# Optimization experiments

Hardware: AMD Instinct MI355X
Metric: run time of the kernel (lower is better)

Reference implementation:

```python
import jax, jax.numpy as jnp
import numpy as np

D_EMBED = 768
N_HEADS = 12
HEAD_DIM = D_EMBED // N_HEADS


def setup_inputs() -> dict:
    key = jax.random.key(0)
    ks = jax.random.split(key, 9)
    B, T, C = 4, 2048, D_EMBED
    s = 1.0 / np.sqrt(C)
    return {
        "x": jax.random.normal(ks[0], (B, T, C), dtype=jnp.float32),
        "Wq": jax.random.normal(ks[1], (C, C), dtype=jnp.float32) * s,
        "bq": jnp.zeros((C,), dtype=jnp.float32),
        "Wk": jax.random.normal(ks[2], (C, C), dtype=jnp.float32) * s,
        "bk": jnp.zeros((C,), dtype=jnp.float32),
        "Wv": jax.random.normal(ks[3], (C, C), dtype=jnp.float32) * s,
        "bv": jnp.zeros((C,), dtype=jnp.float32),
        "Wo": jax.random.normal(ks[4], (C, C), dtype=jnp.float32) * s,
        "bo": jnp.zeros((C,), dtype=jnp.float32),
    }


def reference(x, Wq, bq, Wk, bk, Wv, bv, Wo, bo):
    B, T, C = x.shape
    H, D = N_HEADS, HEAD_DIM
    # projections -> [B, H, T, D]
    q = (x @ Wq + bq).reshape(B, T, H, D).transpose(0, 2, 1, 3)
    k = (x @ Wk + bk).reshape(B, T, H, D).transpose(0, 2, 1, 3)
    v = (x @ Wv + bv).reshape(B, T, H, D).transpose(0, 2, 1, 3)
    # full attention matrix [B, H, T, T] (faithful to manual implementation)
    scores = jnp.einsum('bhqd,bhkd->bhqk', q, k) / jnp.sqrt(jnp.float32(D))
    causal = jnp.tril(jnp.ones((T, T), dtype=bool))
    scores = jnp.where(causal, scores, jnp.float32(-jnp.inf))
    weights = jax.nn.softmax(scores, axis=-1)
    out = jnp.einsum('bhqk,bhkd->bhqd', weights, v)
    out = out.transpose(0, 2, 1, 3).reshape(B, T, C)
    return out @ Wo + bo
```

## Files before the change

kernel.cpp:

```cpp
#include <hip/hip_runtime.h>

#define T_LEN 2048
#define C_DIM 768
#define NH 12
#define HD 64
#define B_SZ 4
#define M_ROWS (B_SZ * T_LEN)
#define WSZ (C_DIM * C_DIM)
#define CH 520

typedef __bf16 bf16x8 __attribute__((ext_vector_type(8)));
typedef float f32x4 __attribute__((ext_vector_type(4)));
typedef float f32x16 __attribute__((ext_vector_type(16)));

__device__ __forceinline__ unsigned short f2bf(float f) {
    union { __bf16 b; unsigned short u; } c;
    c.b = (__bf16)f;
    return c.u;
}

__device__ __forceinline__ float fast_exp2(float x) {
    float r;
    asm("v_exp_f32 %0, %1" : "=v"(r) : "v"(x));
    return r;
}

__device__ __forceinline__ unsigned cvt_pk_bf16(float a, float b) {
    unsigned r;
    asm("v_cvt_pk_bf16_f32 %0, %1, %2" : "=v"(r) : "v"(a), "v"(b));
    return r;
}

__device__ __forceinline__ void perml32_swap(unsigned& a, unsigned& b) {
    asm("v_permlane32_swap_b32 %0, %1" : "+v"(a), "+v"(b));
}

__device__ __forceinline__ void gl2lds16(const void* g, void* l) {
    __builtin_amdgcn_global_load_lds(
        (const __attribute__((address_space(1))) unsigned int*)g,
        (__attribute__((address_space(3))) unsigned int*)l, 16, 0, 0);
}

__global__ __launch_bounds__(256) void conv_x(const float* __restrict__ x,
                                              unsigned short* __restrict__ xb)
{
    const int i = blockIdx.x * 256 + threadIdx.x;
    float4 v = ((const float4*)x)[i];
    ushort4 o;
    o.x = f2bf(v.x); o.y = f2bf(v.y); o.z = f2bf(v.z); o.w = f2bf(v.w);
    ((ushort4*)xb)[i] = o;
}

__global__ __launch_bounds__(256) void conv_wt(
    const float* __restrict__ W0, const float* __restrict__ W1,
    const float* __restrict__ W2, const float* __restrict__ W3,
    unsigned short* __restrict__ WtAll)
{
    __shared__ float tile[32][33];
    const int z = blockIdx.z;
    const float* W = (z == 0) ? W0 : (z == 1) ? W1 : (z == 2) ? W2 : W3;
    unsigned short* out = WtAll + (size_t)z * WSZ;
    const int k0 = blockIdx.x * 32, n0 = blockIdx.y * 32;
    const int r = threadIdx.x >> 3, c4 = (threadIdx.x & 7) * 4;
    float4 v = *(const float4*)&W[(size_t)(k0 + r) * C_DIM + n0 + c4];
    tile[r][c4 + 0] = v.x;
    tile[r][c4 + 1] = v.y;
    tile[r][c4 + 2] = v.z;
    tile[r][c4 + 3] = v.w;
    __syncthreads();
    ushort4 o;
    o.x = f2bf(tile[c4 + 0][r]);
    o.y = f2bf(tile[c4 + 1][r]);
    o.z = f2bf(tile[c4 + 2][r]);
    o.w = f2bf(tile[c4 + 3][r]);
    *(ushort4*)&out[(size_t)(n0 + r) * C_DIM + k0 + c4] = o;
}

template <int BN, int MODE>
__global__ __launch_bounds__(256, 2) void gemm_tile(
    const unsigned short* __restrict__ A, const unsigned short* __restrict__ Wt,
    const float* __restrict__ b0, const float* __restrict__ b1,
    const float* __restrict__ b2,
    unsigned short* __restrict__ qg, unsigned short* __restrict__ kg,
    unsigned short* __restrict__ vtg, float* __restrict__ outF)
{
    constexpr int NFC = BN / 32;
    constexpr int NY = (MODE == 0 ? 2304 : 768) / BN;
    __shared__ __align__(16) unsigned short As[2][128 * 64];
    __shared__ __align__(16) unsigned short Bs[2][BN * 64];

    const int tid = threadIdx.x;
    const int lane = tid & 63, w = tid >> 6;
    const int L15 = lane & 15, quad = lane >> 4;
    const int wm = w >> 1, wn = w & 1;

    const int raw = blockIdx.x;
    const int xcd = raw & 7, i = raw >> 3;
    const int mx = xcd * 8 + i / NY;
    const int ny = i % NY;

    const int lr = lane >> 3;
    const int lg8 = (lane & 7) ^ lr;
    const size_t aBase = (size_t)(mx * 128 + w * 8 + lr) * C_DIM + lg8 * 8;
    const size_t bBase = (size_t)(ny * BN + w * 8 + lr) * C_DIM + lg8 * 8;

    auto stage = [&](int kt, int buf) {
        const size_t ko = (size_t)kt * 64;
#pragma unroll
        for (int c = 0; c < 4; c++)
            gl2lds16(&A[aBase + (size_t)c * 32 * C_DIM + ko],
                     &As[buf][(c * 32 + w * 8) * 64]);
#pragma unroll
        for (int c = 0; c < BN / 32; c++)
            gl2lds16(&Wt[bBase + (size_t)c * 32 * C_DIM + ko],
                     &Bs[buf][(c * 32 + w * 8) * 64]);
    };

    const int sg0 = (quad ^ (L15 & 7)) * 16;
    const int sg1 = ((4 + quad) ^ (L15 & 7)) * 16;
    const int aRowB = (wm * 64 + L15) * 128;
    const int bRowB = (wn * (BN / 2) + L15) * 128;

    f32x4 acc[4][NFC];
#pragma unroll
    for (int fr = 0; fr < 4; fr++)
#pragma unroll
        for (int fc = 0; fc < NFC; fc++) acc[fr][fc] = 0.0f;

    stage(0, 0);
    __syncthreads();

    for (int kt = 0; kt < 12; kt++) {
        const int cur = kt & 1;
        if (kt < 11) stage(kt + 1, cur ^ 1);
        const char* Ac = (const char*)As[cur];
        const char* Bc = (const char*)Bs[cur];
        bf16x8 av[4][2], bv[NFC][2];
#pragma unroll
        for (int fr = 0; fr < 4; fr++)
#pragma unroll
            for (int kh = 0; kh < 2; kh++)
                av[fr][kh] = *(const bf16x8*)(Ac + aRowB + fr * 2048 + (kh ? sg1 : sg0));
#pragma unroll
        for (int fc = 0; fc < NFC; fc++)
#pragma unroll
            for (int kh = 0; kh < 2; kh++)
                bv[fc][kh] = *(const bf16x8*)(Bc + bRowB + fc * 2048 + (kh ? sg1 : sg0));
        __builtin_amdgcn_s_setprio(1);
#pragma unroll
        for (int fr = 0; fr < 4; fr++)
#pragma unroll
            for (int fc = 0; fc < NFC; fc++)
#pragma unroll
                for (int kh = 0; kh < 2; kh++)
                    acc[fr][fc] = __builtin_amdgcn_mfma_f32_16x16x32_bf16(
                        av[fr][kh], bv[fc][kh], acc[fr][fc], 0, 0, 0);
        __builtin_amdgcn_s_setprio(0);
        __syncthreads();
    }

    if (MODE == 0) {
        const int z = (ny * BN) / 768;
        const float* bias = (z == 0) ? b0 : (z == 1) ? b1 : b2;
        const float qs = (z == 0) ? 0.18033688011112042f : 1.0f;
#pragma unroll
        for (int fc = 0; fc < NFC; fc++) {
            const int n = ny * BN + wn * (BN / 2) + fc * 16 + L15;
            const int nl = n - z * 768;
            const int h = nl >> 6, d = nl & 63;
            const float bn = bias[nl];
#pragma unroll
            for (int fr = 0; fr < 4; fr++) {
                const int mB = mx * 128 + wm * 64 + fr * 16 + quad * 4;
                const int b = mB >> 11, tB = mB & (T_LEN - 1);
                if (z < 2) {
                    unsigned short* o = z ? kg : qg;
#pragma unroll
                    for (int r = 0; r < 4; r++)
                        o[(((size_t)(b * NH + h)) * T_LEN + tB + r) * HD + d] =
                            f2bf((acc[fr][fc][r] + bn) * qs);
                } else {
                    ushort4 o4;
                    o4.x = f2bf(acc[fr][fc][0] + bn);
                    o4.y = f2bf(acc[fr][fc][1] + bn);
                    o4.z = f2bf(acc[fr][fc][2] + bn);
                    o4.w = f2bf(acc[fr][fc][3] + bn);
                    *(ushort4*)&vtg[(((size_t)(b * NH + h)) * HD + d) * T_LEN + tB] = o4;
                }
            }
        }
    } else {
#pragma unroll
        for (int fc = 0; fc < NFC; fc++) {
            const int n = ny * BN + wn * (BN / 2) + fc * 16 + L15;
            const float bn = b0[n];
#pragma unroll
            for (int fr = 0; fr < 4; fr++) {
                const int mB = mx * 128 + wm * 64 + fr * 16 + quad * 4;
#pragma unroll
                for (int r = 0; r < 4; r++)
                    outF[(size_t)(mB + r) * C_DIM + n] = acc[fr][fc][r] + bn;
            }
        }
    }
}

__global__ __launch_bounds__(256, 4) void attn_mfma(
    const unsigned short* __restrict__ qg, const unsigned short* __restrict__ kg,
    const unsigned short* __restrict__ vtg, unsigned short* __restrict__ attb)
{
    __shared__ __align__(16) unsigned short Ks[2][8 * CH];
    __shared__ __align__(16) unsigned short Vs[2][8 * CH];
    const int tid = threadIdx.x;
    const int lane = tid & 63, w = tid >> 6;
    const int L15 = lane & 15, L31 = lane & 31;
    const int quad = lane >> 4, r4 = (lane >> 4) & 1, r5 = lane >> 5;

    const int n = blockIdx.x;
    const int bh = n % (B_SZ * NH);
    const int m = n / (B_SZ * NH);
    const int qi = (m & 1) ? (m >> 1) : (15 - (m >> 1));
    const size_t base = (size_t)bh * T_LEN * HD;
    const int q0 = qi * 128;
    const int nk = 2 * qi + 2;
    const int qrow = q0 + w * 32 + L31;

    bf16x8 qf[4];
#pragma unroll
    for (int kc = 0; kc < 4; kc++)
        qf[kc] = *(const bf16x8*)&qg[base + (size_t)qrow * HD + kc * 16 + r5 * 8];

    f32x16 accO[2];
#pragma unroll
    for (int md = 0; md < 2; md++) accO[md] = 0.0f;
    f32x4 lacc = 0.0f;

    auto stage = [&](int kt, int buf) {
        const int ktb = kt * 64;
        gl2lds16(&kg[base + (size_t)(ktb + w * 16 + L15) * HD + quad * 8],
                 &Ks[buf][(2 * w) * CH]);
        gl2lds16(&kg[base + (size_t)(ktb + w * 16 + L15) * HD + 32 + quad * 8],
                 &Ks[buf][(2 * w + 1) * CH]);
        gl2lds16(&vtg[base + (size_t)(w * 16 + L15) * T_LEN + ktb + quad * 8],
                 &Vs[buf][(2 * w) * CH]);
        gl2lds16(&vtg[base + (size_t)(w * 16 + L15) * T_LEN + ktb + 32 + quad * 8],
                 &Vs[buf][(2 * w + 1) * CH]);
    };

    stage(0, 0);
    __syncthreads();

    const int qmaxw = q0 + w * 32 + 31;
    const int qminw = q0 + w * 32;

    for (int kt = 0; kt < nk; kt++) {
        const int cur = kt & 1;
        if (kt + 1 < nk) stage(kt + 1, cur ^ 1);
        const int ktb = kt * 64;
        if (ktb <= qmaxw) {
            f32x16 sa[2];
#pragma unroll
            for (int mi = 0; mi < 2; mi++) {
                sa[mi] = 0.0f;
#pragma unroll
                for (int kc = 0; kc < 4; kc++) {
                    const int ck = mi * 4 + r4 * 2 + (kc >> 1);
                    const int slot = L15 + 16 * ((kc & 1) * 2 + r5);
                    bf16x8 kf = *(const bf16x8*)&Ks[cur][ck * CH + slot * 8];
                    sa[mi] = __builtin_amdgcn_mfma_f32_32x32x16_bf16(
                        kf, qf[kc], sa[mi], 0, 0, 0);
                }
            }
            const bool needmask = (ktb + 63 > qminw);
            bf16x8 pfrag[4];
#pragma unroll
            for (int mi = 0; mi < 2; mi++) {
                float e[16];
#pragma unroll
                for (int g = 0; g < 4; g++) {
#pragma unroll
                    for (int rr = 0; rr < 4; rr++) {
                        float s = sa[mi][g * 4 + rr];
                        if (needmask) {
                            const int key = ktb + mi * 32 + 8 * g + 4 * r5 + rr;
                            s = (key <= qrow) ? s : -1e30f;
                        }
                        e[g * 4 + rr] = fast_exp2(s);
                        lacc[rr] += e[g * 4 + rr];
                    }
                }
#pragma unroll
                for (int h = 0; h < 2; h++) {
                    unsigned a0 = cvt_pk_bf16(e[8 * h + 0], e[8 * h + 1]);
                    unsigned a1 = cvt_pk_bf16(e[8 * h + 2], e[8 * h + 3]);
                    unsigned b0 = cvt_pk_bf16(e[8 * h + 4], e[8 * h + 5]);
                    unsigned b1 = cvt_pk_bf16(e[8 * h + 6], e[8 * h + 7]);
                    perml32_swap(a0, b0);
                    perml32_swap(a1, b1);
                    union { unsigned u[4]; bf16x8 v; } pf;
                    pf.u[0] = a0; pf.u[1] = a1; pf.u[2] = b0; pf.u[3] = b1;
                    pfrag[2 * mi + h] = pf.v;
                }
            }
#pragma unroll
            for (int md = 0; md < 2; md++) {
#pragma unroll
                for (int kc = 0; kc < 4; kc++) {
                    const int cv = md * 4 + r4 * 2 + (kc >> 1);
                    const int slot = L15 + 16 * ((kc & 1) * 2 + r5);
                    bf16x8 vf = *(const bf16x8*)&Vs[cur][cv * CH + slot * 8];
                    accO[md] = __builtin_amdgcn_mfma_f32_32x32x16_bf16(
                        vf, pfrag[kc], accO[md], 0, 0, 0);
                }
            }
        }
        __syncthreads();
    }

    const float l = (lacc[0] + lacc[1]) + (lacc[2] + lacc[3]);
    const float lt = l + __shfl_xor(l, 32, 64);
    const float inv = __builtin_amdgcn_rcpf(lt);
    const int b = bh / NH, h = bh % NH;
    const size_t orow = ((size_t)(b * T_LEN + qrow)) * C_DIM + h * HD;
#pragma unroll
    for (int md = 0; md < 2; md++) {
#pragma unroll
        for (int g = 0; g < 4; g++) {
            uint2 wv;
            wv.x = (unsigned)f2bf(accO[md][g * 4 + 0] * inv) |
                   ((unsigned)f2bf(accO[md][g * 4 + 1] * inv) << 16);
            wv.y = (unsigned)f2bf(accO[md][g * 4 + 2] * inv) |
                   ((unsigned)f2bf(accO[md][g * 4 + 3] * inv) << 16);
            *(uint2*)&attb[orow + md * 32 + 8 * g + 4 * r5] = wv;
        }
    }
}

extern "C" void kernel_launch(void* const* d_in, const int* in_sizes, int n_in,
                              void* d_out, int out_size, void* d_ws, size_t ws_size,
                              hipStream_t stream)
{
    const float* x  = (const float*)d_in[0];
    const float* Wq = (const float*)d_in[1];
    const float* bq = (const float*)d_in[2];
    const float* Wk = (const float*)d_in[3];
    const float* bk = (const float*)d_in[4];
    const float* Wv = (const float*)d_in[5];
    const float* bv = (const float*)d_in[6];
    const float* Wo = (const float*)d_in[7];
    const float* bo = (const float*)d_in[8];
    float* out = (float*)d_out;

    const size_t nMC = (size_t)M_ROWS * C_DIM;
    unsigned short* xb   = (unsigned short*)d_ws;
    unsigned short* Wt   = xb + nMC;
    unsigned short* qg   = Wt + 4 * (size_t)WSZ;
    unsigned short* kg   = qg + nMC;
    unsigned short* vtg  = kg + nMC;
    unsigned short* attb = vtg + nMC;

    conv_x<<<(int)(nMC / 1024), 256, 0, stream>>>(x, xb);
    conv_wt<<<dim3(24, 24, 4), 256, 0, stream>>>(Wq, Wk, Wv, Wo, Wt);
    gemm_tile<192, 0><<<768, 256, 0, stream>>>(xb, Wt, bq, bk, bv,
                                               qg, kg, vtg, nullptr);
    attn_mfma<<<16 * B_SZ * NH, 256, 0, stream>>>(qg, kg, vtg, attb);
    gemm_tile<96, 1><<<512, 256, 0, stream>>>(attb, Wt + 3 * (size_t)WSZ,
                                              bo, bo, bo, nullptr, nullptr,
                                              nullptr, out);
}
```

Before: 213.0 us.

## Split causal attention into balanced key-range chunks with combine pass; use 32x32 MFMA GEMM

Attention work for long query blocks is split across several key-range segments via static tables, so each of the 1920 blocks has similar work. Partial unnormalized outputs and row sums go into scratch that reuses the output buffer and the no-longer-needed bf16 x buffer, and a separate combine kernel sums them and normalizes. The causal diagonal tile now skips the upper-half QK and PV MFMAs. The projection GEMMs switch from 16x16x32 to 32x32x16 MFMA tiles with new LDS indexing. This adds an extra kernel launch plus scratch traffic, and partials are rounded to bf16 before summation.

New measurement: 212.2 us. Within noise of the previous version (-0.4%).

```diff
diff --git a/kernel.cpp b/kernel.cpp
--- a/kernel.cpp
+++ b/kernel.cpp
@@ -39,6 +39,13 @@
     __builtin_amdgcn_global_load_lds(
         (const __attribute__((address_space(1))) unsigned int*)g,
         (__attribute__((address_space(3))) unsigned int*)l, 16, 0, 0);
+}
+
+__device__ __forceinline__ float bf_lo(unsigned u) {
+    union { unsigned u; float f; } c; c.u = u << 16; return c.f;
+}
+__device__ __forceinline__ float bf_hi(unsigned u) {
+    union { unsigned u; float f; } c; c.u = u & 0xFFFF0000u; return c.f;
 }
 
 __global__ __launch_bounds__(256) void conv_x(const float* __restrict__ x,
@@ -84,15 +91,17 @@
     unsigned short* __restrict__ qg, unsigned short* __restrict__ kg,
     unsigned short* __restrict__ vtg, float* __restrict__ outF)
 {
-    constexpr int NFC = BN / 32;
+    constexpr int NT = 3;
+    constexpr int MT = (MODE == 0) ? 2 : 1;
     constexpr int NY = (MODE == 0 ? 2304 : 768) / BN;
     __shared__ __align__(16) unsigned short As[2][128 * 64];
     __shared__ __align__(16) unsigned short Bs[2][BN * 64];
 
     const int tid = threadIdx.x;
     const int lane = tid & 63, w = tid >> 6;
-    const int L15 = lane & 15, quad = lane >> 4;
-    const int wm = w >> 1, wn = w & 1;
+    const int L31 = lane & 31, r5 = lane >> 5;
+    const int wm = (MODE == 0) ? (w >> 1) : w;
+    const int wn = (MODE == 0) ? (w & 1) : 0;
 
     const int raw = blockIdx.x;
     const int xcd = raw & 7, i = raw >> 3;
@@ -116,16 +125,15 @@
                      &Bs[buf][(c * 32 + w * 8) * 64]);
     };
 
-    const int sg0 = (quad ^ (L15 & 7)) * 16;
-    const int sg1 = ((4 + quad) ^ (L15 & 7)) * 16;
-    const int aRowB = (wm * 64 + L15) * 128;
-    const int bRowB = (wn * (BN / 2) + L15) * 128;
-
-    f32x4 acc[4][NFC];
-#pragma unroll
-    for (int fr = 0; fr < 4; fr++)
-#pragma unroll
-        for (int fc = 0; fc < NFC; fc++) acc[fr][fc] = 0.0f;
+    const int ax7 = L31 & 7;
+    const int aRowB = (wm * (MT * 32) + L31) * 128;
+    const int bRowB = (wn * 96 + L31) * 128;
+
+    f32x16 acc[MT][NT];
+#pragma unroll
+    for (int mt = 0; mt < MT; mt++)
+#pragma unroll
+        for (int nt = 0; nt < NT; nt++) acc[mt][nt] = 0.0f;
 
     stage(0, 0);
     __syncthreads();
@@ -135,26 +143,28 @@
         if (kt < 11) stage(kt + 1, cur ^ 1);
         const char* Ac = (const char*)As[cur];
         const char* Bc = (const char*)Bs[cur];
-        bf16x8 av[4][2], bv[NFC][2];
-#pragma unroll
-        for (int fr = 0; fr < 4; fr++)
-#pragma unroll
-            for (int kh = 0; kh < 2; kh++)
-                av[fr][kh] = *(const bf16x8*)(Ac + aRowB + fr * 2048 + (kh ? sg1 : sg0));
-#pragma unroll
-        for (int fc = 0; fc < NFC; fc++)
-#pragma unroll
-            for (int kh = 0; kh < 2; kh++)
-                bv[fc][kh] = *(const bf16x8*)(Bc + bRowB + fc * 2048 + (kh ? sg1 : sg0));
+        bf16x8 av[MT][4], bv[NT][4];
+#pragma unroll
+        for (int mt = 0; mt < MT; mt++)
+#pragma unroll
+            for (int ks = 0; ks < 4; ks++)
+                av[mt][ks] = *(const bf16x8*)(Ac + aRowB + mt * 32 * 128 +
+                                              (((2 * ks + r5) ^ ax7) * 16));
+#pragma unroll
+        for (int nt = 0; nt < NT; nt++)
+#pragma unroll
+            for (int ks = 0; ks < 4; ks++)
+                bv[nt][ks] = *(const bf16x8*)(Bc + bRowB + nt * 32 * 128 +
+                                              (((2 * ks + r5) ^ ax7) * 16));
         __builtin_amdgcn_s_setprio(1);
 #pragma unroll
-        for (int fr = 0; fr < 4; fr++)
-#pragma unroll
-            for (int fc = 0; fc < NFC; fc++)
-#pragma unroll
-                for (int kh = 0; kh < 2; kh++)
-                    acc[fr][fc] = __builtin_amdgcn_mfma_f32_16x16x32_bf16(
-                        av[fr][kh], bv[fc][kh], acc[fr][fc], 0, 0, 0);
+        for (int ks = 0; ks < 4; ks++)
+#pragma unroll
+            for (int mt = 0; mt < MT; mt++)
+#pragma unroll
+                for (int nt = 0; nt < NT; nt++)
+                    acc[mt][nt] = __builtin_amdgcn_mfma_f32_32x32x16_bf16(
+                        av[mt][ks], bv[nt][ks], acc[mt][nt], 0, 0, 0);
         __builtin_amdgcn_s_setprio(0);
         __syncthreads();
     }
@@ -164,51 +174,75 @@
         const float* bias = (z == 0) ? b0 : (z == 1) ? b1 : b2;
         const float qs = (z == 0) ? 0.18033688011112042f : 1.0f;
 #pragma unroll
-        for (int fc = 0; fc < NFC; fc++) {
-            const int n = ny * BN + wn * (BN / 2) + fc * 16 + L15;
+        for (int nt = 0; nt < NT; nt++) {
+            const int n = ny * BN + wn * 96 + nt * 32 + L31;
             const int nl = n - z * 768;
             const int h = nl >> 6, d = nl & 63;
             const float bn = bias[nl];
 #pragma unroll
-            for (int fr = 0; fr < 4; fr++) {
-                const int mB = mx * 128 + wm * 64 + fr * 16 + quad * 4;
-                const int b = mB >> 11, tB = mB & (T_LEN - 1);
+            for (int mt = 0; mt < MT; mt++) {
+                const int mB = mx * 128 + wm * (MT * 32) + mt * 32;
+                const int b = mB >> 11, tBb = mB & (T_LEN - 1);
                 if (z < 2) {
                     unsigned short* o = z ? kg : qg;
 #pragma unroll
-                    for (int r = 0; r < 4; r++)
-                        o[(((size_t)(b * NH + h)) * T_LEN + tB + r) * HD + d] =
-                            f2bf((acc[fr][fc][r] + bn) * qs);
+                    for (int reg = 0; reg < 16; reg++) {
+                        const int t = tBb + (reg & 3) + 8 * (reg >> 2) + 4 * r5;
+                        o[(((size_t)(b * NH + h)) * T_LEN + t) * HD + d] =
+                            f2bf((acc[mt][nt][reg] + bn) * qs);
+                    }
                 } else {
-                    ushort4 o4;
-                    o4.x = f2bf(acc[fr][fc][0] + bn);
-                    o4.y = f2bf(acc[fr][fc][1] + bn);
-                    o4.z = f2bf(acc[fr][fc][2] + bn);
-                    o4.w = f2bf(acc[fr][fc][3] + bn);
-                    *(ushort4*)&vtg[(((size_t)(b * NH + h)) * HD + d) * T_LEN + tB] = o4;
+#pragma unroll
+                    for (int g = 0; g < 4; g++) {
+                        const int t0 = tBb + 8 * g + 4 * r5;
+                        ushort4 o4;
+                        o4.x = f2bf(acc[mt][nt][g * 4 + 0] + bn);
+                        o4.y = f2bf(acc[mt][nt][g * 4 + 1] + bn);
+                        o4.z = f2bf(acc[mt][nt][g * 4 + 2] + bn);
+                        o4.w = f2bf(acc[mt][nt][g * 4 + 3] + bn);
+                        *(ushort4*)&vtg[(((size_t)(b * NH + h)) * HD + d) * T_LEN + t0] = o4;
+                    }
                 }
             }
         }
     } else {
 #pragma unroll
-        for (int fc = 0; fc < NFC; fc++) {
-            const int n = ny * BN + wn * (BN / 2) + fc * 16 + L15;
+        for (int nt = 0; nt < NT; nt++) {
+            const int n = ny * BN + nt * 32 + L31;
             const float bn = b0[n];
 #pragma unroll
-            for (int fr = 0; fr < 4; fr++) {
-                const int mB = mx * 128 + wm * 64 + fr * 16 + quad * 4;
-#pragma unroll
-                for (int r = 0; r < 4; r++)
-                    outF[(size_t)(mB + r) * C_DIM + n] = acc[fr][fc][r] + bn;
+            for (int reg = 0; reg < 16; reg++) {
+                const int m = mx * 128 + w * 32 + (reg & 3) + 8 * (reg >> 2) + 4 * r5;
+                outF[(size_t)m * C_DIM + n] = acc[0][nt][reg] + bn;
             }
         }
     }
 }
 
-__global__ __launch_bounds__(256, 4) void attn_mfma(
+__global__ __launch_bounds__(256, 4) void attn_part(
     const unsigned short* __restrict__ qg, const unsigned short* __restrict__ kg,
-    const unsigned short* __restrict__ vtg, unsigned short* __restrict__ attb)
-{
+    const unsigned short* __restrict__ vtg, unsigned short* __restrict__ attb,
+    float* __restrict__ pOa, unsigned short* __restrict__ pOb,
+    float* __restrict__ pL)
+{
+    static const unsigned char Uqs[40] = {
+        15,15,15,15,14,14,11,11,11,10, 7, 7, 3,
+        14,14,13,13,13,13,12,12,10,10, 9, 9, 6, 6,
+        12,12, 9, 8, 8, 8, 5, 5, 2, 4, 4, 1, 0};
+    static const unsigned char Uk0[40] = {
+         0, 8,16,24, 0, 8, 0, 8,16, 0, 0, 8, 0,
+        16,23, 0, 7,14,21, 0, 7, 8,15, 0, 7, 0, 7,
+        14,20,14, 0, 6,12, 0, 6, 0, 0, 5, 0, 0};
+    static const unsigned char Uk1[40] = {
+         8,16,24,32, 8,16, 8,16,24, 8, 8,16, 8,
+        23,30, 7,14,21,28, 7,14,15,22, 7,14, 7,14,
+        20,26,20, 6,12,18, 6,12, 6, 5,10, 4, 2};
+    static const unsigned char Useg[40] = {
+         0, 1, 2, 3, 0, 1, 0, 1, 2, 0, 0, 1, 0,
+         2, 3, 0, 1, 2, 3, 0, 1, 1, 2, 0, 1, 0, 1,
+         2, 3, 2, 0, 1, 2, 0, 1, 0, 0, 1, 0, 0};
+    static const unsigned char SB[12] = {0,2,4,6,8,11,14,17,20,24,28,32};
+
     __shared__ __align__(16) unsigned short Ks[2][8 * CH];
     __shared__ __align__(16) unsigned short Vs[2][8 * CH];
     const int tid = threadIdx.x;
@@ -218,11 +252,11 @@
 
     const int n = blockIdx.x;
     const int bh = n % (B_SZ * NH);
-    const int m = n / (B_SZ * NH);
-    const int qi = (m & 1) ? (m >> 1) : (15 - (m >> 1));
+    const int u = n / (B_SZ * NH);
+    const int qs = Uqs[u];
+    const int k0 = Uk0[u], k1 = Uk1[u];
     const size_t base = (size_t)bh * T_LEN * HD;
-    const int q0 = qi * 128;
-    const int nk = 2 * qi + 2;
+    const int q0 = qs * 128;
     const int qrow = q0 + w * 32 + L31;
 
     bf16x8 qf[4];
@@ -247,93 +281,172 @@
                  &Vs[buf][(2 * w + 1) * CH]);
     };
 
-    stage(0, 0);
+    stage(k0, 0);
     __syncthreads();
 
     const int qmaxw = q0 + w * 32 + 31;
     const int qminw = q0 + w * 32;
 
-    for (int kt = 0; kt < nk; kt++) {
-        const int cur = kt & 1;
-        if (kt + 1 < nk) stage(kt + 1, cur ^ 1);
+    for (int kt = k0; kt < k1; kt++) {
+        const int cur = (kt - k0) & 1;
+        if (kt + 1 < k1) stage(kt + 1, cur ^ 1);
         const int ktb = kt * 64;
         if (ktb <= qmaxw) {
-            f32x16 sa[2];
-#pragma unroll
-            for (int mi = 0; mi < 2; mi++) {
-                sa[mi] = 0.0f;
-#pragma unroll
-                for (int kc = 0; kc < 4; kc++) {
-                    const int ck = mi * 4 + r4 * 2 + (kc >> 1);
-                    const int slot = L15 + 16 * ((kc & 1) * 2 + r5);
-                    bf16x8 kf = *(const bf16x8*)&Ks[cur][ck * CH + slot * 8];
-                    sa[mi] = __builtin_amdgcn_mfma_f32_32x32x16_bf16(
-                        kf, qf[kc], sa[mi], 0, 0, 0);
-                }
-            }
+            const bool hi = (ktb + 32 <= qmaxw);
             const bool needmask = (ktb + 63 > qminw);
             bf16x8 pfrag[4];
+            f32x16 sa[2];
 #pragma unroll
             for (int mi = 0; mi < 2; mi++) {
-                float e[16];
-#pragma unroll
-                for (int g = 0; g < 4; g++) {
-#pragma unroll
-                    for (int rr = 0; rr < 4; rr++) {
-                        float s = sa[mi][g * 4 + rr];
-                        if (needmask) {
-                            const int key = ktb + mi * 32 + 8 * g + 4 * r5 + rr;
-                            s = (key <= qrow) ? s : -1e30f;
+                if (mi == 0 || hi) {
+                    sa[mi] = 0.0f;
+                    __builtin_amdgcn_s_setprio(1);
+#pragma unroll
+                    for (int kc = 0; kc < 4; kc++) {
+                        const int ck = mi * 4 + r4 * 2 + (kc >> 1);
+                        const int slot = L15 + 16 * ((kc & 1) * 2 + r5);
+                        bf16x8 kf = *(const bf16x8*)&Ks[cur][ck * CH + slot * 8];
+                        sa[mi] = __builtin_amdgcn_mfma_f32_32x32x16_bf16(
+                            kf, qf[kc], sa[mi], 0, 0, 0);
+                    }
+                    __builtin_amdgcn_s_setprio(0);
+                    float e[16];
+#pragma unroll
+                    for (int g = 0; g < 4; g++) {
+#pragma unroll
+                        for (int rr = 0; rr < 4; rr++) {
+                            float s = sa[mi][g * 4 + rr];
+                            if (needmask) {
+                                const int key = ktb + mi * 32 + 8 * g + 4 * r5 + rr;
+                                s = (key <= qrow) ? s : -1e30f;
+                            }
+                            e[g * 4 + rr] = fast_exp2(s);
+                            lacc[rr] += e[g * 4 + rr];
                         }
-                        e[g * 4 + rr] = fast_exp2(s);
-                        lacc[rr] += e[g * 4 + rr];
+                    }
+#pragma unroll
+                    for (int h = 0; h < 2; h++) {
+                        unsigned a0 = cvt_pk_bf16(e[8 * h + 0], e[8 * h + 1]);
+                        unsigned a1 = cvt_pk_bf16(e[8 * h + 2], e[8 * h + 3]);
+                        unsigned b0 = cvt_pk_bf16(e[8 * h + 4], e[8 * h + 5]);
+                        unsigned b1 = cvt_pk_bf16(e[8 * h + 6], e[8 * h + 7]);
+                        perml32_swap(a0, b0);
+                        perml32_swap(a1, b1);
+                        union { unsigned u[4]; bf16x8 v; } pf;
+                        pf.u[0] = a0; pf.u[1] = a1; pf.u[2] = b0; pf.u[3] = b1;
+                        pfrag[2 * mi + h] = pf.v;
                     }
                 }
-#pragma unroll
-                for (int h = 0; h < 2; h++) {
-                    unsigned a0 = cvt_pk_bf16(e[8 * h + 0], e[8 * h + 1]);
-                    unsigned a1 = cvt_pk_bf16(e[8 * h + 2], e[8 * h + 3]);
-                    unsigned b0 = cvt_pk_bf16(e[8 * h + 4], e[8 * h + 5]);
-                    unsigned b1 = cvt_pk_bf16(e[8 * h + 6], e[8 * h + 7]);
-                    perml32_swap(a0, b0);
-                    perml32_swap(a1, b1);
-                    union { unsigned u[4]; bf16x8 v; } pf;
-                    pf.u[0] = a0; pf.u[1] = a1; pf.u[2] = b0; pf.u[3] = b1;
-                    pfrag[2 * mi + h] = pf.v;
+            }
+            __builtin_amdgcn_s_setprio(1);
+#pragma unroll
+            for (int md = 0; md < 2; md++) {
+#pragma unroll
+                for (int kc = 0; kc < 4; kc++) {
+                    if (kc < 2 || hi) {
+                        const int cv = md * 4 + r4 * 2 + (kc >> 1);
+                        const int slot = L15 + 16 * ((kc & 1) * 2 + r5);
+                        bf16x8 vf = *(const bf16x8*)&Vs[cur][cv * CH + slot * 8];
+                        accO[md] = __builtin_amdgcn_mfma_f32_32x32x16_bf16(
+                            vf, pfrag[kc], accO[md], 0, 0, 0);
+                    }
                 }
             }
-#pragma unroll
-            for (int md = 0; md < 2; md++) {
-#pragma unroll
-                for (int kc = 0; kc < 4; kc++) {
-                    const int cv = md * 4 + r4 * 2 + (kc >> 1);
-                    const int slot = L15 + 16 * ((kc & 1) * 2 + r5);
-                    bf16x8 vf = *(const bf16x8*)&Vs[cur][cv * CH + slot * 8];
-                    accO[md] = __builtin_amdgcn_mfma_f32_32x32x16_bf16(
-                        vf, pfrag[kc], accO[md], 0, 0, 0);
-                }
-            }
+            __builtin_amdgcn_s_setprio(0);
         }
         __syncthreads();
     }
 
     const float l = (lacc[0] + lacc[1]) + (lacc[2] + lacc[3]);
+    if (qs < 4) {
+        const float lt = l + __shfl_xor(l, 32, 64);
+        const float inv = __builtin_amdgcn_rcpf(lt);
+        const int b = bh / NH, h = bh % NH;
+        const size_t orow = ((size_t)(b * T_LEN + qrow)) * C_DIM + h * HD;
+#pragma unroll
+        for (int md = 0; md < 2; md++) {
+#pragma unroll
+            for (int g = 0; g < 4; g++) {
+                uint2 wv;
+                wv.x = cvt_pk_bf16(accO[md][g * 4 + 0] * inv, accO[md][g * 4 + 1] * inv);
+                wv.y = cvt_pk_bf16(accO[md][g * 4 + 2] * inv, accO[md][g * 4 + 3] * inv);
+                *(uint2*)&attb[orow + md * 32 + 8 * g + 4 * r5] = wv;
+            }
+        }
+    } else {
+        const int slot = bh * 36 + SB[qs - 4] + Useg[u];
+        char* sp = (slot < 1536) ? ((char*)pOa + (size_t)slot * 16384)
+                                 : ((char*)pOb + (size_t)(slot - 1536) * 16384);
+        unsigned uu[16];
+#pragma unroll
+        for (int md = 0; md < 2; md++)
+#pragma unroll
+            for (int g = 0; g < 4; g++) {
+                uu[md * 8 + g * 2 + 0] = cvt_pk_bf16(accO[md][g * 4 + 0], accO[md][g * 4 + 1]);
+                uu[md * 8 + g * 2 + 1] = cvt_pk_bf16(accO[md][g * 4 + 2], accO[md][g * 4 + 3]);
+            }
+        uint4* dst = (uint4*)sp + tid * 4;
+#pragma unroll
+        for (int p = 0; p < 4; p++) {
+            uint4 q;
+            q.x = uu[p * 4 + 0]; q.y = uu[p * 4 + 1];
+            q.z = uu[p * 4 + 2]; q.w = uu[p * 4 + 3];
+            dst[p] = q;
+        }
+        pL[(size_t)slot * 256 + tid] = l;
+    }
+}
+
+__global__ __launch_bounds__(256) void attn_comb(
+    const float* __restrict__ pOa, const unsigned short* __restrict__ pOb,
+    const float* __restrict__ pL, unsigned short* __restrict__ attb)
+{
+    static const unsigned char SB[12] = {0,2,4,6,8,11,14,17,20,24,28,32};
+    const int tid = threadIdx.x, s = blockIdx.x;
+    const int lane = tid & 63, w = tid >> 6;
+    const int r5 = lane >> 5, L31 = lane & 31;
+    const int bh = s / 12, qi = 4 + s % 12;
+    const int nseg = (qi < 8) ? 2 : ((qi < 12) ? 3 : 4);
+    const int slot0 = bh * 36 + SB[qi - 4];
+
+    float v[32];
+#pragma unroll
+    for (int i = 0; i < 32; i++) v[i] = 0.0f;
+    float l = 0.0f;
+
+    for (int seg = 0; seg < 4; seg++) {
+        if (seg < nseg) {
+            const int slot = slot0 + seg;
+            const char* sp = (slot < 1536)
+                ? ((const char*)pOa + (size_t)slot * 16384)
+                : ((const char*)pOb + (size_t)(slot - 1536) * 16384);
+            const uint4* src = (const uint4*)sp + tid * 4;
+#pragma unroll
+            for (int p = 0; p < 4; p++) {
+                uint4 q = src[p];
+                v[p * 8 + 0] += bf_lo(q.x); v[p * 8 + 1] += bf_hi(q.x);
+                v[p * 8 + 2] += bf_lo(q.y); v[p * 8 + 3] += bf_hi(q.y);
+                v[p * 8 + 4] += bf_lo(q.z); v[p * 8 + 5] += bf_hi(q.z);
+                v[p * 8 + 6] += bf_lo(q.w); v[p * 8 + 7] += bf_hi(q.w);
+            }
+            l += pL[(size_t)slot * 256 + tid];
+        }
+    }
+
     const float lt = l + __shfl_xor(l, 32, 64);
     const float inv = __builtin_amdgcn_rcpf(lt);
+    const int qrow = qi * 128 + w * 32 + L31;
     const int b = bh / NH, h = bh % NH;
     const size_t orow = ((size_t)(b * T_LEN + qrow)) * C_DIM + h * HD;
 #pragma unroll
-    for (int md = 0; md < 2; md++) {
+    for (int md = 0; md < 2; md++)
 #pragma unroll
         for (int g = 0; g < 4; g++) {
             uint2 wv;
-            wv.x = (unsigned)f2bf(accO[md][g * 4 + 0] * inv) |
-                   ((unsigned)f2bf(accO[md][g * 4 + 1] * inv) << 16);
-            wv.y = (unsigned)f2bf(accO[md][g * 4 + 2] * inv) |
-                   ((unsigned)f2bf(accO[md][g * 4 + 3] * inv) << 16);
+            wv.x = cvt_pk_bf16(v[md * 16 + g * 4 + 0] * inv, v[md * 16 + g * 4 + 1] * inv);
+            wv.y = cvt_pk_bf16(v[md * 16 + g * 4 + 2] * inv, v[md * 16 + g * 4 + 3] * inv);
             *(uint2*)&attb[orow + md * 32 + 8 * g + 4 * r5] = wv;
         }
-    }
 }
 
 extern "C" void kernel_launch(void* const* d_in, const int* in_sizes, int n_in,
@@ -358,12 +471,15 @@
     unsigned short* kg   = qg + nMC;
     unsigned short* vtg  = kg + nMC;
     unsigned short* attb = vtg + nMC;
+    float* pL = (float*)((char*)xb + 6 * 1024 * 1024);
 
     conv_x<<<(int)(nMC / 1024), 256, 0, stream>>>(x, xb);
     conv_wt<<<dim3(24, 24, 4), 256, 0, stream>>>(Wq, Wk, Wv, Wo, Wt);
     gemm_tile<192, 0><<<768, 256, 0, stream>>>(xb, Wt, bq, bk, bv,
                                                qg, kg, vtg, nullptr);
-    attn_mfma<<<16 * B_SZ * NH, 256, 0, stream>>>(qg, kg, vtg, attb);
+    attn_part<<<40 * B_SZ * NH, 256, 0, stream>>>(qg, kg, vtg, attb,
+                                                  out, xb, pL);
+    attn_comb<<<576, 256, 0, stream>>>(out, xb, pL, attb);
     gemm_tile<96, 1><<<512, 256, 0, stream>>>(attb, Wt + 3 * (size_t)WSZ,
                                               bo, bo, bo, nullptr, nullptr,
                                               nullptr, out);
```
